# Kernel tuning notes

Hardware: AMD Instinct MI355X
Metric: run time of the kernel (lower is better)

## Reference

```python
import jax, jax.numpy as jnp
import numpy as np

B, S, D = 4, 1024, 1024
H, DK, DH = 16, 64, 64  # num_heads, key_size, head_size
NEG = 1e12


def setup_inputs() -> dict:
    key = jax.random.key(0)
    ks = jax.random.split(key, 16)
    scale = 0.02
    inp = {
        'q': jax.random.normal(ks[0], (B, S, D), jnp.float32),
        'k': jax.random.normal(ks[1], (B, S, D), jnp.float32),
        'v': jax.random.normal(ks[2], (B, S, D), jnp.float32),
        'v_mask': jax.random.randint(ks[3], (B, S), 0, 2, jnp.int32),
        'q_mask': jax.random.randint(ks[4], (B, S), 0, 2, jnp.int32),
        # causal attention mask (float, 1 = keep)
        'a_mask': jnp.tril(jnp.ones((S, S), jnp.float32))[None, None, :, :],
        'Wq': jax.random.normal(ks[5], (D, H * DK), jnp.float32) * scale,
        'bq': jnp.zeros((H * DK,), jnp.float32),
        'Wk': jax.random.normal(ks[6], (D, H * DK), jnp.float32) * scale,
        'bk': jnp.zeros((H * DK,), jnp.float32),
        'Wv': jax.random.normal(ks[7], (D, H * DH), jnp.float32) * scale,
        'bv': jnp.zeros((H * DH,), jnp.float32),
        'Wo': jax.random.normal(ks[8], (H * DH, H * DH), jnp.float32) * scale,
        'bo': jnp.zeros((H * DH,), jnp.float32),
    }
    return inp


def reference(q, k, v, v_mask, q_mask, a_mask, Wq, bq, Wk, bk, Wv, bv, Wo, bo):
    b, sq, _ = q.shape
    sk = k.shape[1]
    qw = (jnp.einsum('bsd,de->bse', q, Wq) + bq).reshape(b, sq, H, DK)
    kw = (jnp.einsum('bsd,de->bse', k, Wk) + bk).reshape(b, sk, H, DK)
    vw = (jnp.einsum('bsd,de->bse', v, Wv) + bv).reshape(b, sk, H, DH)
    # scores [b, h, sq, sk]
    a = jnp.einsum('bjhd,bkhd->bhjk', qw, kw) / jnp.sqrt(jnp.float32(DK))
    vm = v_mask.astype(jnp.float32)  # [b, sk]
    a = a - (1.0 - vm)[:, None, None, :] * NEG  # sequence_masking mode='add'
    a = a - (1.0 - a_mask) * NEG                # attention mask
    p = jax.nn.softmax(a, axis=-1)
    o = jnp.einsum('bhjk,bkhd->bjhd', p, vw).reshape(b, sq, H * DH)
    o = jnp.einsum('bse,ef->bsf', o, Wo) + bo
    qm = q_mask.astype(jnp.float32)
    o = o * qm[:, :, None]  # sequence_masking mode='mul'
    return o
```

## Files before the change

kernel.cpp:

```cpp
#include <hip/hip_runtime.h>
#include <cstdint>
#include <cstddef>

typedef unsigned short u16;
using short8 = __attribute__((ext_vector_type(8))) short;
using f32x4  = __attribute__((ext_vector_type(4))) float;

constexpr int Sc = 1024;
constexpr float PEN = 60.0f;

__device__ __forceinline__ u16 f2bf(float f) {
  union { float f; uint32_t u; } v; v.f = f;
  return (u16)((v.u + 0x7fffu + ((v.u >> 16) & 1u)) >> 16);
}

__device__ __forceinline__ void gload_lds16(const u16* g, u16* l) {
  __builtin_amdgcn_global_load_lds(
      (const __attribute__((address_space(1))) uint32_t*)g,
      (__attribute__((address_space(3))) uint32_t*)l, 16, 0, 0);
}

__device__ __forceinline__ f32x4 mfma16(short8 a, short8 b, f32x4 c) {
  return __builtin_amdgcn_mfma_f32_16x16x32_bf16(a, b, c, 0, 0, 0);
}

__global__ __launch_bounds__(256) void prep(
    const float* __restrict__ q, const float* __restrict__ k,
    const float* __restrict__ v, u16* __restrict__ qb, u16* __restrict__ kb,
    u16* __restrict__ vb, const float* __restrict__ W0,
    const float* __restrict__ W1, const float* __restrict__ W2,
    const float* __restrict__ W3, u16* __restrict__ D0, u16* __restrict__ D1,
    u16* __restrict__ D2, u16* __restrict__ D3) {
  const int y = blockIdx.y;
  if (y < 3) {
    const float* src = y == 0 ? q : y == 1 ? k : v;
    u16* dst = y == 0 ? qb : y == 1 ? kb : vb;
    int i = blockIdx.x * 256 + threadIdx.x;
    float4 a = ((const float4*)src)[2 * i];
    float4 b = ((const float4*)src)[2 * i + 1];
    u16 t[8] = {f2bf(a.x), f2bf(a.y), f2bf(a.z), f2bf(a.w),
                f2bf(b.x), f2bf(b.y), f2bf(b.z), f2bf(b.w)};
    ((uint4*)dst)[i] = *(const uint4*)t;
  } else {
    if (blockIdx.x >= 1024) return;
    const int z = y - 3;
    const float* W = z == 0 ? W0 : z == 1 ? W1 : z == 2 ? W2 : W3;
    u16* WT = z == 0 ? D0 : z == 1 ? D1 : z == 2 ? D2 : D3;
    __shared__ float t[32][33];
    int bx = (blockIdx.x & 31) * 32, by = (blockIdx.x >> 5) * 32;
    int tx = threadIdx.x & 31, ty = threadIdx.x >> 5;
    for (int i = 0; i < 32; i += 8)
      t[ty + i][tx] = W[(size_t)(by + ty + i) * 1024 + bx + tx];
    __syncthreads();
    for (int i = 0; i < 32; i += 8)
      WT[(size_t)(bx + ty + i) * 1024 + by + tx] = f2bf(t[tx][ty + i]);
  }
}

__global__ __launch_bounds__(256, 6) void gemm_qkv(
    const u16* __restrict__ qb, const u16* __restrict__ kb,
    const u16* __restrict__ vb, const u16* __restrict__ BT,
    const float* __restrict__ bq, const float* __restrict__ bk,
    const float* __restrict__ bv, u16* __restrict__ QW, u16* __restrict__ KW,
    u16* __restrict__ VTg) {
  const int bid = blockIdx.x;
  const int xcd = bid & 7, local = bid >> 3;
  const int mp = local & 3, nbi = local >> 2;
  const int m0 = (xcd * 4 + mp) * 128, n0 = nbi * 64;
  const int seg = nbi >> 4;
  const u16* A    = seg == 0 ? qb : seg == 1 ? kb : vb;
  const float* bias = seg == 0 ? bq : seg == 1 ? bk : bv;

  __shared__ u16 As0[128 * 32], As1[128 * 32];
  __shared__ u16 Bs0[64 * 32], Bs1[64 * 32];

  const int t = threadIdx.x, w = t >> 6, lane = t & 63;
  const int q4 = lane >> 4, lm = lane & 15;
  const int wm = (w >> 1) * 64, wn = (w & 1) * 32;
  const int srow = lane >> 2, p = lane & 3;
  const int cf = q4 ^ ((lm >> 2) & 3);

  const int rbA0 = (w * 2) * 16, rbA1 = (w * 2 + 1) * 16, rbB = w * 16;
  const int rowA0 = rbA0 + srow, rowA1 = rbA1 + srow, rowB = rbB + srow;
  const int cA0 = p ^ ((rowA0 >> 2) & 3), cA1 = p ^ ((rowA1 >> 2) & 3);
  const int cB = p ^ ((rowB >> 2) & 3);
  const u16* pa0 = &A[(size_t)(m0 + rowA0) * 1024 + cA0 * 8];
  const u16* pa1 = &A[(size_t)(m0 + rowA1) * 1024 + cA1 * 8];
  const u16* pb  = &BT[(size_t)(n0 + rowB) * 1024 + cB * 8];

  f32x4 acc[4][2] = {};

  auto stage = [&](u16* as, u16* bs) {
    gload_lds16(pa0, as + rbA0 * 32);
    gload_lds16(pa1, as + rbA1 * 32);
    gload_lds16(pb, bs + rbB * 32);
    pa0 += 32; pa1 += 32; pb += 32;
  };
  auto compute = [&](const u16* as, const u16* bs) {
    short8 af[4], bf[2];
    for (int mi = 0; mi < 4; ++mi)
      af[mi] = *(const short8*)&as[(wm + mi * 16 + lm) * 32 + cf * 8];
    for (int ni = 0; ni < 2; ++ni)
      bf[ni] = *(const short8*)&bs[(wn + ni * 16 + lm) * 32 + cf * 8];
    for (int mi = 0; mi < 4; ++mi)
      for (int ni = 0; ni < 2; ++ni)
        acc[mi][ni] = mfma16(af[mi], bf[ni], acc[mi][ni]);
  };

  stage(As0, Bs0);
  for (int it = 0; it < 16; ++it) {
    __syncthreads();
    stage(As1, Bs1);
    compute(As0, Bs0);
    __syncthreads();
    if (it < 15) stage(As0, Bs0);
    compute(As1, Bs1);
  }

  if (seg < 2) {
    u16* C = seg == 0 ? QW : KW;
    for (int mi = 0; mi < 4; ++mi)
      for (int ni = 0; ni < 2; ++ni)
        for (int r = 0; r < 4; ++r) {
          int row = m0 + wm + mi * 16 + q4 * 4 + r;
          int col = (n0 + wn + ni * 16 + lm) & 1023;
          C[(size_t)row * 1024 + col] = f2bf(acc[mi][ni][r] + bias[col]);
        }
  } else {
    for (int mi = 0; mi < 4; ++mi)
      for (int ni = 0; ni < 2; ++ni) {
        int row0 = m0 + wm + mi * 16 + q4 * 4;
        int col = (n0 + wn + ni * 16 + lm) & 1023;
        float bv4 = bias[col];
        u16 o4[4];
        for (int r = 0; r < 4; ++r) o4[r] = f2bf(acc[mi][ni][r] + bv4);
        *(uint2*)&VTg[(size_t)col * 4096 + row0] = *(const uint2*)o4;
      }
  }
}

__global__ __launch_bounds__(256, 4) void gemm_out(
    const u16* __restrict__ A, const u16* __restrict__ BT,
    const float* __restrict__ bias, const int* __restrict__ qmask,
    float* __restrict__ Cf) {
  const int bid = blockIdx.x;
  const int xcd = bid & 7, local = bid >> 3;
  const int mp = local & 7, nb = local >> 3;
  const int m0 = (xcd * 8 + mp) * 64, n0 = nb * 64;

  __shared__ u16 As0[64 * 32], As1[64 * 32];
  __shared__ u16 Bs0[64 * 32], Bs1[64 * 32];
  const int t = threadIdx.x, w = t >> 6, lane = t & 63;
  const int q4 = lane >> 4, lm = lane & 15;
  const int wm = (w >> 1) * 32, wn = (w & 1) * 32;
  const int srow = lane >> 2, p = lane & 3;
  const int cf = q4 ^ ((lm >> 2) & 3);

  const int rb = w * 16;
  const int rowS = rb + srow;
  const int cS = p ^ ((rowS >> 2) & 3);
  const u16* pa = &A[(size_t)(m0 + rowS) * 1024 + cS * 8];
  const u16* pb = &BT[(size_t)(n0 + rowS) * 1024 + cS * 8];

  f32x4 acc[2][2] = {};

  auto stage = [&](u16* as, u16* bs) {
    gload_lds16(pa, as + rb * 32);
    gload_lds16(pb, bs + rb * 32);
    pa += 32; pb += 32;
  };
  auto compute = [&](const u16* as, const u16* bs) {
    short8 af[2], bf[2];
    for (int mi = 0; mi < 2; ++mi)
      af[mi] = *(const short8*)&as[(wm + mi * 16 + lm) * 32 + cf * 8];
    for (int ni = 0; ni < 2; ++ni)
      bf[ni] = *(const short8*)&bs[(wn + ni * 16 + lm) * 32 + cf * 8];
    for (int mi = 0; mi < 2; ++mi)
      for (int ni = 0; ni < 2; ++ni)
        acc[mi][ni] = mfma16(af[mi], bf[ni], acc[mi][ni]);
  };

  stage(As0, Bs0);
  for (int it = 0; it < 16; ++it) {
    __syncthreads();
    stage(As1, Bs1);
    compute(As0, Bs0);
    __syncthreads();
    if (it < 15) stage(As0, Bs0);
    compute(As1, Bs1);
  }

  for (int mi = 0; mi < 2; ++mi)
    for (int ni = 0; ni < 2; ++ni)
      for (int r = 0; r < 4; ++r) {
        int row = m0 + wm + mi * 16 + q4 * 4 + r;
        int col = n0 + wn + ni * 16 + lm;
        Cf[(size_t)row * 1024 + col] =
            (acc[mi][ni][r] + bias[col]) * (float)qmask[row];
      }
}

__global__ __launch_bounds__(64, 4) void attn(
    const u16* __restrict__ QW, const u16* __restrict__ KW,
    const u16* __restrict__ VTg, const int* __restrict__ vmask,
    u16* __restrict__ O) {
  const int bid = blockIdx.x;
  const int qtidx = bid >> 8;
  const int qt = qtidx == 0 ? 0 : 16 - qtidx;
  const int rem = bid & 255;
  const int quarter = 3 - (rem >> 6);
  const int bh = rem & 63;
  const int b = bh >> 4, h = bh & 15;
  const int lane = threadIdx.x;
  const int q4 = lane >> 4, lm = lane & 15;

  __shared__ u16 Ks[2][32 * 64];
  __shared__ u16 P[16 * 40];
  __shared__ unsigned char penb[1024];

  {
    const int4* vmp = (const int4*)(vmask + b * 1024);
    for (int j = 0; j < 4; ++j) {
      int4 vm = vmp[4 * lane + j];
      unsigned char m4[4] = {
          (unsigned char)(vm.x == 0), (unsigned char)(vm.y == 0),
          (unsigned char)(vm.z == 0), (unsigned char)(vm.w == 0)};
      *(unsigned int*)&penb[16 * lane + 4 * j] = *(const unsigned int*)m4;
    }
  }
  int any = 0;
  for (int i = lane; i <= qt * 64; i += 64) any |= (penb[i] == 0);
  const int ext = (__ballot(any) == 0);
  const int T = 2 * qt + (quarter >> 1);
  const int kend = ext ? 31 : T;

  const int R = qt * 64 + quarter * 16;
  short8 qf[2];
  {
    const u16* qp = &QW[(size_t)(b * Sc + R + lm) * 1024 + h * 64];
    qf[0] = *(const short8*)&qp[q4 * 8];
    qf[1] = *(const short8*)&qp[32 + q4 * 8];
    for (int fi = 0; fi < 2; ++fi)
      for (int i = 0; i < 8; ++i) {
        u16 x = (u16)qf[fi][i];
        int e = (x >> 7) & 0xff;
        qf[fi][i] = (short)(e > 3 ? (u16)(x - 0x180) : (u16)(x & 0x8000));
      }
  }

  float l_run[4] = {};
  f32x4 oacc[4] = {};
  const int qrow00 = R + q4 * 4;

  const u16* Kbase = &KW[(size_t)(b * Sc) * 1024 + h * 64];
  const u16* Vbase = &VTg[(size_t)(h * 64) * 4096 + b * Sc];

  const int r0 = lane >> 3, pos = lane & 7, ch = pos ^ r0;
  auto stageK = [&](int kt, int buf) {
    for (int j = 0; j < 4; ++j) {
      int row = j * 8 + r0;
      gload_lds16(Kbase + (size_t)(kt * 32 + row) * 1024 + ch * 8,
                  &Ks[buf][j * 512]);
    }
  };

  stageK(0, 0);
  for (int kt = 0; kt <= kend; ++kt) {
    const int buf = kt & 1;
    short8 vf[4];
#pragma unroll
    for (int ni = 0; ni < 4; ++ni)
      vf[ni] = *(const short8*)(Vbase + (size_t)(ni * 16 + lm) * 4096 +
                                kt * 32 + q4 * 8);
    if (kt < kend) {
      stageK(kt + 1, buf ^ 1);
      asm volatile("s_waitcnt vmcnt(8)" ::: "memory");
    } else {
      asm volatile("s_waitcnt vmcnt(4)" ::: "memory");
    }
    __builtin_amdgcn_sched_barrier(0);

    const int mode = kt > T ? 2 : (kt == T ? 1 : 0);
    f32x4 sacc[2] = {};
    __builtin_amdgcn_s_setprio(1);
#pragma unroll
    for (int ni = 0; ni < 2; ++ni) {
      int row = ni * 16 + lm;
      short8 kf0 = *(const short8*)&Ks[buf][row * 64 + ((q4 ^ (lm & 7)) * 8)];
      short8 kf1 = *(const short8*)&Ks[buf][row * 64 + (((4 + q4) ^ (lm & 7)) * 8)];
      sacc[ni] = mfma16(qf[0], kf0, sacc[ni]);
      sacc[ni] = mfma16(qf[1], kf1, sacc[ni]);
    }
    __builtin_amdgcn_s_setprio(0);

#pragma unroll
    for (int ni = 0; ni < 2; ++ni) {
      int key = kt * 32 + ni * 16 + lm;
      float pen = penb[key] ? PEN : 0.0f;
      if (mode == 2) pen += PEN;
#pragma unroll
      for (int r = 0; r < 4; ++r) {
        float x = sacc[ni][r] - pen;
        if (mode == 1 && key > qrow00 + r) x -= PEN;
        float pv = __expf(x);
        l_run[r] += pv;
        P[(q4 * 4 + r) * 40 + ni * 16 + lm] = f2bf(pv);
      }
    }
    short8 pf = *(const short8*)&P[lm * 40 + q4 * 8];
    __builtin_amdgcn_s_setprio(1);
#pragma unroll
    for (int ni = 0; ni < 4; ++ni)
      oacc[ni] = mfma16(pf, vf[ni], oacc[ni]);
    __builtin_amdgcn_s_setprio(0);
  }

  for (int r = 0; r < 4; ++r) {
    float l = l_run[r];
    for (int off = 1; off < 16; off <<= 1) l += __shfl_xor(l, off, 64);
    l_run[r] = 1.0f / l;
  }
  for (int ni = 0; ni < 4; ++ni)
    for (int r = 0; r < 4; ++r) {
      int row = b * Sc + qrow00 + r;
      O[(size_t)row * 1024 + h * 64 + ni * 16 + lm] =
          f2bf(oacc[ni][r] * l_run[r]);
    }
}

extern "C" void kernel_launch(void* const* d_in, const int* in_sizes, int n_in,
                              void* d_out, int out_size, void* d_ws, size_t ws_size,
                              hipStream_t stream) {
  (void)in_sizes; (void)n_in; (void)out_size; (void)ws_size;
  const float* q  = (const float*)d_in[0];
  const float* k  = (const float*)d_in[1];
  const float* v  = (const float*)d_in[2];
  const int* vmask = (const int*)d_in[3];
  const int* qmask = (const int*)d_in[4];
  const float* Wq = (const float*)d_in[6];
  const float* bq = (const float*)d_in[7];
  const float* Wk = (const float*)d_in[8];
  const float* bk = (const float*)d_in[9];
  const float* Wv = (const float*)d_in[10];
  const float* bv = (const float*)d_in[11];
  const float* Wo = (const float*)d_in[12];
  const float* bo = (const float*)d_in[13];

  char* ws = (char*)d_ws;
  u16* WT3 = (u16*)ws;
  u16* WoT = (u16*)(ws + 6291456);
  u16* QW  = (u16*)(ws + 8388608);
  u16* KW  = (u16*)(ws + 16777216);
  u16* VTg = (u16*)(ws + 25165824);
  u16* Oat = (u16*)(ws + 33554432);
  u16* qb = (u16*)d_out;
  u16* kb = (u16*)d_out + 4194304;
  u16* vb = Oat;

  dim3 tb(256);
  prep<<<dim3(2048, 7), tb, 0, stream>>>(q, k, v, qb, kb, vb, Wq, Wk, Wv, Wo,
                                         WT3, WT3 + 1048576, WT3 + 2097152,
                                         WoT);
  gemm_qkv<<<dim3(1536), tb, 0, stream>>>(qb, kb, vb, WT3, bq, bk, bv, QW, KW,
                                          VTg);
  attn<<<dim3(4096), dim3(64), 0, stream>>>(QW, KW, VTg, vmask, Oat);
  gemm_out<<<dim3(1024), tb, 0, stream>>>(Oat, WoT, bo, qmask, (float*)d_out);
}
```

Baseline: 232.5 us.

## Pair complementary causal query strips per attention block to balance and share K/V

```diff
diff --git a/kernel.cpp b/kernel.cpp
--- a/kernel.cpp
+++ b/kernel.cpp
@@ -200,19 +200,21 @@
       }
 }
 
-__global__ __launch_bounds__(64, 4) void attn(
+__global__ __launch_bounds__(64, 3) void attn(
     const u16* __restrict__ QW, const u16* __restrict__ KW,
     const u16* __restrict__ VTg, const int* __restrict__ vmask,
     u16* __restrict__ O) {
   const int bid = blockIdx.x;
-  const int qtidx = bid >> 8;
-  const int qt = qtidx == 0 ? 0 : 16 - qtidx;
-  const int rem = bid & 255;
-  const int quarter = 3 - (rem >> 6);
-  const int bh = rem & 63;
+  const int X = bid >> 8;
+  const int rA = (bid >> 6) & 3, rB = 3 - rA;
+  const int bh = bid & 63;
   const int b = bh >> 4, h = bh & 15;
   const int lane = threadIdx.x;
   const int q4 = lane >> 4, lm = lane & 15;
+
+  const int qtA = X, qtB = 15 - X;
+  const int TA = 2 * qtA + (rA >> 1), TB = 2 * qtB + (rB >> 1);
+  const int RA = qtA * 64 + rA * 16, RB = qtB * 64 + rB * 16;
 
   __shared__ u16 Ks[2][32 * 64];
   __shared__ u16 P[16 * 40];
@@ -228,15 +230,18 @@
       *(unsigned int*)&penb[16 * lane + 4 * j] = *(const unsigned int*)m4;
     }
   }
-  int any = 0;
-  for (int i = lane; i <= qt * 64; i += 64) any |= (penb[i] == 0);
-  const int ext = (__ballot(any) == 0);
-  const int T = 2 * qt + (quarter >> 1);
-  const int kend = ext ? 31 : T;
-
-  const int R = qt * 64 + quarter * 16;
-  short8 qf[2];
-  {
+  int anyA = 0, anyB = 0;
+  for (int i = lane; i <= qtB * 64; i += 64) {
+    int un = (penb[i] == 0);
+    if (i <= qtA * 64) anyA |= un;
+    anyB |= un;
+  }
+  const int extA = (__ballot(anyA) == 0);
+  const int extB = (__ballot(anyB) == 0);
+  const int kend = (extA || extB) ? 31 : TB;
+
+  short8 qfA[2], qfB[2];
+  auto loadQ = [&](int R, short8 (&qf)[2]) {
     const u16* qp = &QW[(size_t)(b * Sc + R + lm) * 1024 + h * 64];
     qf[0] = *(const short8*)&qp[q4 * 8];
     qf[1] = *(const short8*)&qp[32 + q4 * 8];
@@ -246,11 +251,13 @@
         int e = (x >> 7) & 0xff;
         qf[fi][i] = (short)(e > 3 ? (u16)(x - 0x180) : (u16)(x & 0x8000));
       }
-  }
-
-  float l_run[4] = {};
-  f32x4 oacc[4] = {};
-  const int qrow00 = R + q4 * 4;
+  };
+  loadQ(RA, qfA);
+  loadQ(RB, qfB);
+
+  float lA[4] = {}, lB[4] = {};
+  f32x4 oaccA[4] = {}, oaccB[4] = {};
+  const int qr0A = RA + q4 * 4, qr0B = RB + q4 * 4;
 
   const u16* Kbase = &KW[(size_t)(b * Sc) * 1024 + h * 64];
   const u16* Vbase = &VTg[(size_t)(h * 64) * 4096 + b * Sc];
@@ -262,6 +269,43 @@
       gload_lds16(Kbase + (size_t)(kt * 32 + row) * 1024 + ch * 8,
                   &Ks[buf][j * 512]);
     }
+  };
+
+  auto strip = [&](const short8 (&qf)[2], f32x4 (&oacc)[4], float (&lr)[4],
+                   int Tdiag, int qr0, int kt, int buf, const short8 (&vf)[4]) {
+    const int mode = kt > Tdiag ? 2 : (kt == Tdiag ? 1 : 0);
+    f32x4 sacc[2] = {};
+    __builtin_amdgcn_s_setprio(1);
+#pragma unroll
+    for (int ni = 0; ni < 2; ++ni) {
+      int row = ni * 16 + lm;
+      short8 kf0 = *(const short8*)&Ks[buf][row * 64 + ((q4 ^ (lm & 7)) * 8)];
+      short8 kf1 = *(const short8*)&Ks[buf][row * 64 + (((4 + q4) ^ (lm & 7)) * 8)];
+      sacc[ni] = mfma16(qf[0], kf0, sacc[ni]);
+      sacc[ni] = mfma16(qf[1], kf1, sacc[ni]);
+    }
+    __builtin_amdgcn_s_setprio(0);
+
+#pragma unroll
+    for (int ni = 0; ni < 2; ++ni) {
+      int key = kt * 32 + ni * 16 + lm;
+      float pen = penb[key] ? PEN : 0.0f;
+      if (mode == 2) pen += PEN;
+#pragma unroll
+      for (int r = 0; r < 4; ++r) {
+        float x = sacc[ni][r] - pen;
+        if (mode == 1 && key > qr0 + r) x -= PEN;
+        float pv = __expf(x);
+        lr[r] += pv;
+        P[(q4 * 4 + r) * 40 + ni * 16 + lm] = f2bf(pv);
+      }
+    }
+    short8 pf = *(const short8*)&P[lm * 40 + q4 * 8];
+    __builtin_amdgcn_s_setprio(1);
+#pragma unroll
+    for (int ni = 0; ni < 4; ++ni)
+      oacc[ni] = mfma16(pf, vf[ni], oacc[ni]);
+    __builtin_amdgcn_s_setprio(0);
   };
 
   stageK(0, 0);
@@ -280,52 +324,27 @@
     }
     __builtin_amdgcn_sched_barrier(0);
 
-    const int mode = kt > T ? 2 : (kt == T ? 1 : 0);
-    f32x4 sacc[2] = {};
-    __builtin_amdgcn_s_setprio(1);
-#pragma unroll
-    for (int ni = 0; ni < 2; ++ni) {
-      int row = ni * 16 + lm;
-      short8 kf0 = *(const short8*)&Ks[buf][row * 64 + ((q4 ^ (lm & 7)) * 8)];
-      short8 kf1 = *(const short8*)&Ks[buf][row * 64 + (((4 + q4) ^ (lm & 7)) * 8)];
-      sacc[ni] = mfma16(qf[0], kf0, sacc[ni]);
-      sacc[ni] = mfma16(qf[1], kf1, sacc[ni]);
-    }
-    __builtin_amdgcn_s_setprio(0);
-
-#pragma unroll
-    for (int ni = 0; ni < 2; ++ni) {
-      int key = kt * 32 + ni * 16 + lm;
-      float pen = penb[key] ? PEN : 0.0f;
-      if (mode == 2) pen += PEN;
-#pragma unroll
+    if (kt <= TA) strip(qfA, oaccA, lA, TA, qr0A, kt, buf, vf);
+    else if (extA) strip(qfA, oaccA, lA, TA, qr0A, kt, buf, vf);
+    if (kt <= TB) strip(qfB, oaccB, lB, TB, qr0B, kt, buf, vf);
+    else if (extB) strip(qfB, oaccB, lB, TB, qr0B, kt, buf, vf);
+  }
+
+  auto epilogue = [&](f32x4 (&oacc)[4], float (&lr)[4], int qr0) {
+    for (int r = 0; r < 4; ++r) {
+      float l = lr[r];
+      for (int off = 1; off < 16; off <<= 1) l += __shfl_xor(l, off, 64);
+      lr[r] = 1.0f / l;
+    }
+    for (int ni = 0; ni < 4; ++ni)
       for (int r = 0; r < 4; ++r) {
-        float x = sacc[ni][r] - pen;
-        if (mode == 1 && key > qrow00 + r) x -= PEN;
-        float pv = __expf(x);
-        l_run[r] += pv;
-        P[(q4 * 4 + r) * 40 + ni * 16 + lm] = f2bf(pv);
-      }
-    }
-    short8 pf = *(const short8*)&P[lm * 40 + q4 * 8];
-    __builtin_amdgcn_s_setprio(1);
-#pragma unroll
-    for (int ni = 0; ni < 4; ++ni)
-      oacc[ni] = mfma16(pf, vf[ni], oacc[ni]);
-    __builtin_amdgcn_s_setprio(0);
-  }
-
-  for (int r = 0; r < 4; ++r) {
-    float l = l_run[r];
-    for (int off = 1; off < 16; off <<= 1) l += __shfl_xor(l, off, 64);
-    l_run[r] = 1.0f / l;
-  }
-  for (int ni = 0; ni < 4; ++ni)
-    for (int r = 0; r < 4; ++r) {
-      int row = b * Sc + qrow00 + r;
-      O[(size_t)row * 1024 + h * 64 + ni * 16 + lm] =
-          f2bf(oacc[ni][r] * l_run[r]);
-    }
+        int row = b * Sc + qr0 + r;
+        O[(size_t)row * 1024 + h * 64 + ni * 16 + lm] =
+            f2bf(oacc[ni][r] * lr[r]);
+      }
+  };
+  epilogue(oaccA, lA, qr0A);
+  epilogue(oaccB, lB, qr0B);
 }
 
 extern "C" void kernel_launch(void* const* d_in, const int* in_sizes, int n_in,
@@ -363,6 +382,6 @@
                                          WoT);
   gemm_qkv<<<dim3(1536), tb, 0, stream>>>(qb, kb, vb, WT3, bq, bk, bv, QW, KW,
                                           VTg);
-  attn<<<dim3(4096), dim3(64), 0, stream>>>(QW, KW, VTg, vmask, Oat);
+  attn<<<dim3(2048), dim3(64), 0, stream>>>(QW, KW, VTg, vmask, Oat);
   gemm_out<<<dim3(1024), tb, 0, stream>>>(Oat, WoT, bo, qmask, (float*)d_out);
 }
```

After: 229.4 us. Within noise of the previous version (-1.4%).
